# Performance work log

Hardware: AMD Instinct MI355X
Metric: run time of the kernel (lower is better)

## Reference

```python
import jax, jax.numpy as jnp
import numpy as np
import math

EMBED_DIM = 1024
NUM_HEADS = 16
HEAD_DIM = EMBED_DIM // NUM_HEADS


def setup_inputs() -> dict:
    key = jax.random.key(0)
    ks = jax.random.split(key, 5)
    x = jax.random.normal(ks[0], (4, 2048, EMBED_DIM), dtype=jnp.float32)
    # Linear params (torch nn.Linear: y = x @ W.T + b); init scale ~ 1/sqrt(fan_in)
    s = 1.0 / math.sqrt(EMBED_DIM)
    qkv_w = jax.random.uniform(ks[1], (3 * EMBED_DIM, EMBED_DIM), jnp.float32, -s, s)
    qkv_b = jax.random.uniform(ks[2], (3 * EMBED_DIM,), jnp.float32, -s, s)
    proj_w = jax.random.uniform(ks[3], (EMBED_DIM, EMBED_DIM), jnp.float32, -s, s)
    proj_b = jax.random.uniform(ks[4], (EMBED_DIM,), jnp.float32, -s, s)
    return {"x": x, "qkv_w": qkv_w, "qkv_b": qkv_b, "proj_w": proj_w, "proj_b": proj_b}


def reference(x, qkv_w, qkv_b, proj_w, proj_b):
    bsz, num_tokens, dim = x.shape
    qkv = x @ qkv_w.T + qkv_b  # [B, S, 3*D]
    qkv = qkv.reshape(bsz, num_tokens, 3, NUM_HEADS, HEAD_DIM)
    qkv = jnp.transpose(qkv, (2, 0, 3, 1, 4))  # [3, B, H, S, hd]
    q, k, v = qkv[0], qkv[1], qkv[2]
    scale = 1.0 / math.sqrt(HEAD_DIM)
    attn_scores = jnp.einsum('bhqd,bhkd->bhqk', q, k) * scale  # [B, H, S, S]
    attn = jax.nn.softmax(attn_scores, axis=-1)
    out = jnp.einsum('bhqk,bhkd->bhqd', attn, v)  # [B, H, S, hd]
    out = jnp.transpose(out, (0, 2, 1, 3)).reshape(bsz, num_tokens, dim)
    out = out @ proj_w.T + proj_b
    return out
```

## Files before the change

kernel.cpp:

```cpp
#include <hip/hip_runtime.h>
#include <stdint.h>

#define DEVICE static __device__ __forceinline__

typedef __bf16 bf16x8 __attribute__((ext_vector_type(8)));
typedef float f32x4 __attribute__((ext_vector_type(4)));

#define AS1 __attribute__((address_space(1)))
#define AS3 __attribute__((address_space(3)))

DEVICE void g2l16(const void* gptr, void* lptr) {
  __builtin_amdgcn_global_load_lds((AS1 uint32_t*)(uintptr_t)gptr,
                                   (AS3 uint32_t*)(uint32_t)(uintptr_t)lptr,
                                   16, 0, 0);
}

DEVICE float b2f(ushort h) {
  union { uint32_t u; float f; } v;
  v.u = ((uint32_t)h) << 16;
  return v.f;
}
DEVICE ushort f2b(float f) {
  union { float f; uint32_t u; } v;
  v.f = f;
  uint32_t u = v.u;
  return (ushort)((u + 0x7FFFu + ((u >> 16) & 1u)) >> 16);
}

#if defined(__has_builtin) && __has_builtin(__builtin_amdgcn_exp2f)
DEVICE float fast_exp2(float x) { return __builtin_amdgcn_exp2f(x); }
#else
extern "C" __device__ float __ocml_native_exp2_f32(float);
DEVICE float fast_exp2(float x) { return __ocml_native_exp2_f32(x); }
#endif

#define QSCALE 0.1803368801111244f

DEVICE int kperm(int x) {
  return (x & 0x23) | ((x & 0x18) >> 1) | ((x & 0x4) << 2);
}

__global__ void detect_dtype(const ushort* __restrict__ xu, int* __restrict__ flag) {
  __shared__ int bad;
  if (threadIdx.x == 0) bad = 0;
  __syncthreads();
  int mybad = 0;
#pragma unroll
  for (int j = 0; j < 8; ++j) {
    const int i = threadIdx.x * 8 + j;
    const ushort u = xu[2 * i];
    const int e = (u >> 7) & 0xFF;
    if (!(e == 0 || (e >= 96 && e <= 160))) mybad++;
  }
  atomicAdd(&bad, mybad);
  __syncthreads();
  if (threadIdx.x == 0) *flag = (bad > 512) ? 1 : 0;
}

__global__ void convert_bf16(const void* __restrict__ src, ushort* __restrict__ dst,
                             int n, const int* __restrict__ flag) {
  const bool isf32 = (*flag != 0);
  const int n8 = n >> 3;
  for (int i = blockIdx.x * blockDim.x + threadIdx.x; i < n8;
       i += gridDim.x * blockDim.x) {
    ushort pk[8];
    if (isf32) {
      const float4 a = ((const float4*)src)[2 * i];
      const float4 b = ((const float4*)src)[2 * i + 1];
      pk[0] = f2b(a.x); pk[1] = f2b(a.y); pk[2] = f2b(a.z); pk[3] = f2b(a.w);
      pk[4] = f2b(b.x); pk[5] = f2b(b.y); pk[6] = f2b(b.z); pk[7] = f2b(b.w);
      *(uint4*)&dst[8 * i] = *(const uint4*)pk;
    } else {
      *(uint4*)&dst[8 * i] = ((const uint4*)src)[i];
    }
  }
}

template <int MODE, int GN>
__global__ __launch_bounds__(256)
void gemm_bt(const ushort* __restrict__ A, const ushort* __restrict__ W,
             const ushort* __restrict__ bias, ushort* __restrict__ O0,
             ushort* __restrict__ O1, ushort* __restrict__ O2,
             int M, int N, int K, const int* __restrict__ flag)
{
  __shared__ union SM {
    struct { ushort As[128 * 64]; ushort Bs[128 * 64]; } s;
    ushort Ct[128 * 136];
  } sm;

  const int tid = threadIdx.x;
  const int lane = tid & 63;
  const int wave = tid >> 6;
  const int quad = lane >> 4;
  const int lo = lane & 15;

  const int lin = blockIdx.y * gridDim.x + blockIdx.x;
  const int per = GN * gridDim.y;
  const int grp = lin / per;
  const int w   = lin % per;
  const int bxn = grp * GN + (w % GN);
  const int bym = w / GN;
  const int m0 = bym * 128;
  const int n0 = bxn * 128;

  const int wm = (wave >> 1) * 64;
  const int wn = (wave & 1) * 64;

  f32x4 acc[4][4] = {};

  for (int k0 = 0; k0 < K; k0 += 64) {
    __syncthreads();
#pragma unroll
    for (int i = 0; i < 4; ++i) {
      const int c = tid + 256 * i;
      const int row = c >> 3;
      const int kc = (c & 7) << 3;
      g2l16(A + (size_t)(m0 + row) * K + k0 + kc,
            (char*)sm.s.As + ((wave << 6) + (i << 8)) * 16);
      g2l16(W + (size_t)(n0 + row) * K + k0 + kc,
            (char*)sm.s.Bs + ((wave << 6) + (i << 8)) * 16);
    }
    __syncthreads();

#pragma unroll
    for (int ks = 0; ks < 2; ++ks) {
      bf16x8 af[4], bfr[4];
#pragma unroll
      for (int t = 0; t < 4; ++t) {
        af[t]  = *(const bf16x8*)&sm.s.As[(wm + t * 16 + lo) * 64 + ks * 32 + quad * 8];
        bfr[t] = *(const bf16x8*)&sm.s.Bs[(wn + t * 16 + lo) * 64 + ks * 32 + quad * 8];
      }
#pragma unroll
      for (int mt = 0; mt < 4; ++mt)
#pragma unroll
        for (int nt = 0; nt < 4; ++nt)
          acc[mt][nt] = __builtin_amdgcn_mfma_f32_16x16x32_bf16(
              af[mt], bfr[nt], acc[mt][nt], 0, 0, 0);
    }
  }

  if (MODE == 0) {
    const int which = n0 >> 10;
    if (which == 2) {
#pragma unroll
      for (int nt = 0; nt < 4; ++nt) {
        const int n = n0 + wn + nt * 16 + lo;
        const float bv2 = b2f(bias[n]);
        const int h = (n >> 6) & 15;
        const int d = n & 63;
#pragma unroll
        for (int mt = 0; mt < 4; ++mt) {
          const int mb = m0 + wm + mt * 16 + quad * 4;
          const int b = mb >> 11, s0 = mb & 2047;
          ushort pk[4];
#pragma unroll
          for (int r = 0; r < 4; ++r) pk[r] = f2b(acc[mt][nt][r] + bv2);
          *(uint2*)&O2[((size_t)(b * 16 + h) * 64 + d) * 2048 + s0] =
              *(const uint2*)pk;
        }
      }
    } else {
      const float qs = (which == 0) ? QSCALE : 1.0f;
      ushort* __restrict__ dst = (which == 0) ? O0 : O1;
      __syncthreads();
#pragma unroll
      for (int nt = 0; nt < 4; ++nt) {
        const int n = n0 + wn + nt * 16 + lo;
        const float bv2 = b2f(bias[n]);
#pragma unroll
        for (int mt = 0; mt < 4; ++mt)
#pragma unroll
          for (int r = 0; r < 4; ++r)
            sm.Ct[(wm + mt * 16 + quad * 4 + r) * 136 + wn + nt * 16 + lo] =
                f2b((acc[mt][nt][r] + bv2) * qs);
      }
      __syncthreads();
#pragma unroll
      for (int i = 0; i < 8; ++i) {
        const int c = tid + 256 * i;
        const int nch = c & 15;
        const int ml = c >> 4;
        const int n = n0 + nch * 8;
        const int h = (n >> 6) & 15;
        const int d = n & 63;
        const int mg = m0 + ml;
        const int b = mg >> 11;
        int s = mg & 2047;
        if (which == 1) s = (s & ~63) | kperm(s & 63);
        const uint4 val = *(const uint4*)&sm.Ct[ml * 136 + nch * 8];
        *(uint4*)&dst[(((size_t)(b * 16 + h) * 2048 + s) << 6) + d] = val;
      }
    }
  } else {
    const bool f32out = (*flag != 0);
    float* Of = (float*)O0;
#pragma unroll
    for (int nt = 0; nt < 4; ++nt) {
      const int n = n0 + wn + nt * 16 + lo;
      const float bv2 = b2f(bias[n]);
#pragma unroll
      for (int mt = 0; mt < 4; ++mt)
#pragma unroll
        for (int r = 0; r < 4; ++r) {
          const int m = m0 + wm + mt * 16 + quad * 4 + r;
          const float val = acc[mt][nt][r] + bv2;
          if (f32out) Of[(size_t)m * N + n] = val;
          else        O0[(size_t)m * N + n] = f2b(val);
        }
    }
  }
}

__global__ __launch_bounds__(256, 4)
void attn_fwd(const ushort* __restrict__ qp, const ushort* __restrict__ kp,
              const ushort* __restrict__ vp, ushort* __restrict__ o)
{
  __shared__ ushort Qs[128 * 64];
  __shared__ ushort Ks[64 * 64];
  __shared__ ushort Vt[64 * 64];

  const int tid = threadIdx.x;
  const int lane = tid & 63;
  const int wave = tid >> 6;
  const int quad = lane >> 4;
  const int lo = lane & 15;
  const int bh = blockIdx.y;
  const int q0 = blockIdx.x * 128;

  const ushort* Qg = qp + (size_t)bh * 2048 * 64;
  const ushort* Kg = kp + (size_t)bh * 2048 * 64;
  const ushort* Vg = vp + (size_t)bh * 64 * 2048;

#pragma unroll
  for (int i = 0; i < 4; ++i) {
    const int c = tid + 256 * i;
    const int row = c >> 3;
    const int kc = (c & 7) << 3;
    g2l16(Qg + (size_t)(q0 + row) * 64 + kc,
          (char*)Qs + ((wave << 6) + (i << 8)) * 16);
  }
  __syncthreads();

  bf16x8 qf[2][2];
#pragma unroll
  for (int mt = 0; mt < 2; ++mt)
#pragma unroll
    for (int ks = 0; ks < 2; ++ks)
      qf[mt][ks] = *(const bf16x8*)&Qs[(wave * 32 + mt * 16 + lo) * 64 + ks * 32 + quad * 8];

  bf16x8 ones;
#pragma unroll
  for (int j = 0; j < 8; ++j) ones[j] = (__bf16)1.0f;

  f32x4 oacc[2][4] = {};
  f32x4 sumacc[2] = {};

  for (int j0 = 0; j0 < 2048; j0 += 64) {
    __syncthreads();
#pragma unroll
    for (int i = 0; i < 2; ++i) {
      const int c = tid + 256 * i;
      const int row = c >> 3;
      const int kc = (c & 7) << 3;
      g2l16(Kg + (size_t)(j0 + row) * 64 + kc,
            (char*)Ks + ((wave << 6) + (i << 8)) * 16);
      g2l16(Vg + (size_t)row * 2048 + j0 + kc,
            (char*)Vt + ((wave << 6) + (i << 8)) * 16);
    }
    __syncthreads();

    f32x4 sacc[2][4] = {};
#pragma unroll
    for (int ks = 0; ks < 2; ++ks) {
#pragma unroll
      for (int nt = 0; nt < 4; ++nt) {
        const bf16x8 kf = *(const bf16x8*)&Ks[(nt * 16 + lo) * 64 + ks * 32 + quad * 8];
#pragma unroll
        for (int mt = 0; mt < 2; ++mt)
          sacc[mt][nt] = __builtin_amdgcn_mfma_f32_16x16x32_bf16(
              kf, qf[mt][ks], sacc[mt][nt], 0, 0, 0);
      }
    }

    bf16x8 pfr[2][2];
#pragma unroll
    for (int mt = 0; mt < 2; ++mt) {
      float p[4][4];
#pragma unroll
      for (int nt = 0; nt < 4; ++nt)
#pragma unroll
        for (int r = 0; r < 4; ++r)
          p[nt][r] = fast_exp2(sacc[mt][nt][r]);
#pragma unroll
      for (int b = 0; b < 2; ++b)
#pragma unroll
        for (int h = 0; h < 2; ++h)
#pragma unroll
          for (int r = 0; r < 4; ++r)
            pfr[mt][b][4 * h + r] = (__bf16)p[2 * b + h][r];
    }

#pragma unroll
    for (int b = 0; b < 2; ++b) {
#pragma unroll
      for (int mt = 0; mt < 2; ++mt)
        sumacc[mt] = __builtin_amdgcn_mfma_f32_16x16x32_bf16(
            pfr[mt][b], ones, sumacc[mt], 0, 0, 0);
#pragma unroll
      for (int dt = 0; dt < 4; ++dt) {
        const bf16x8 vf = *(const bf16x8*)&Vt[(dt * 16 + lo) * 64 + b * 32 + quad * 8];
#pragma unroll
        for (int mt = 0; mt < 2; ++mt)
          oacc[mt][dt] = __builtin_amdgcn_mfma_f32_16x16x32_bf16(
              pfr[mt][b], vf, oacc[mt][dt], 0, 0, 0);
      }
    }
  }

  const int b_ = bh >> 4;
  const int h = bh & 15;
#pragma unroll
  for (int mt = 0; mt < 2; ++mt) {
#pragma unroll
    for (int r = 0; r < 4; ++r) {
      const float inv = 1.0f / sumacc[mt][r];
      const int srow = q0 + wave * 32 + mt * 16 + quad * 4 + r;
#pragma unroll
      for (int dt = 0; dt < 4; ++dt) {
        o[(((size_t)(b_ * 2048 + srow)) << 10) + h * 64 + dt * 16 + lo] =
            f2b(oacc[mt][dt][r] * inv);
      }
    }
  }
}

extern "C" void kernel_launch(void* const* d_in, const int* in_sizes, int n_in,
                              void* d_out, int out_size, void* d_ws, size_t ws_size,
                              hipStream_t stream) {
  const size_t N_X  = (size_t)4 * 2048 * 1024;
  const size_t N_WQ = (size_t)3072 * 1024;
  const size_t N_BQ = 3072;
  const size_t N_WP = (size_t)1024 * 1024;
  const size_t N_BP = 1024;
  const size_t HSD  = (size_t)64 * 2048 * 64;

  ushort* xb = (ushort*)d_ws;
  ushort* wq = xb + N_X;
  ushort* bq = wq + N_WQ;
  ushort* wp = bq + N_BQ;
  ushort* bp = wp + N_WP;
  ushort* qb = bp + N_BP;
  ushort* kb = qb + HSD;
  ushort* vb = kb + HSD;
  ushort* ab = vb + HSD;
  int* flag  = (int*)(ab + HSD);

  detect_dtype<<<1, 256, 0, stream>>>((const ushort*)d_in[0], flag);
  convert_bf16<<<1024, 256, 0, stream>>>(d_in[0], xb, (int)N_X, flag);
  convert_bf16<<<512, 256, 0, stream>>>(d_in[1], wq, (int)N_WQ, flag);
  convert_bf16<<<2, 256, 0, stream>>>(d_in[2], bq, (int)N_BQ, flag);
  convert_bf16<<<256, 256, 0, stream>>>(d_in[3], wp, (int)N_WP, flag);
  convert_bf16<<<1, 256, 0, stream>>>(d_in[4], bp, (int)N_BP, flag);

  gemm_bt<0, 6><<<dim3(24, 64), dim3(256), 0, stream>>>(
      xb, wq, bq, qb, kb, vb, 8192, 3072, 1024, flag);
  attn_fwd<<<dim3(16, 64), dim3(256), 0, stream>>>(qb, kb, vb, ab);
  gemm_bt<1, 4><<<dim3(8, 64), dim3(256), 0, stream>>>(
      ab, wp, bp, (ushort*)d_out, nullptr, nullptr, 8192, 1024, 1024, flag);
}
```

Measured before the change: 299.3 us.

## Map GEMM tiles to XCD-local rectangles and double attention KV tile

```diff
diff --git a/kernel.cpp b/kernel.cpp
--- a/kernel.cpp
+++ b/kernel.cpp
@@ -76,7 +76,7 @@
   }
 }
 
-template <int MODE, int GN>
+template <int MODE, int RM, int RN>
 __global__ __launch_bounds__(256)
 void gemm_bt(const ushort* __restrict__ A, const ushort* __restrict__ W,
              const ushort* __restrict__ bias, ushort* __restrict__ O0,
@@ -95,13 +95,15 @@
   const int lo = lane & 15;
 
   const int lin = blockIdx.y * gridDim.x + blockIdx.x;
-  const int per = GN * gridDim.y;
-  const int grp = lin / per;
-  const int w   = lin % per;
-  const int bxn = grp * GN + (w % GN);
-  const int bym = w / GN;
-  const int m0 = bym * 128;
-  const int n0 = bxn * 128;
+  const int xcd = lin & 7;
+  const int slot = lin >> 3;
+  const int rects_n = gridDim.x / RN;
+  const int rn = xcd % rects_n;
+  const int rm = xcd / rects_n;
+  const int ml = slot / RN;
+  const int nl = slot % RN;
+  const int m0 = (rm * RM + ml) * 128;
+  const int n0 = (rn * RN + nl) * 128;
 
   const int wm = (wave >> 1) * 64;
   const int wn = (wave & 1) * 64;
@@ -179,15 +181,15 @@
       for (int i = 0; i < 8; ++i) {
         const int c = tid + 256 * i;
         const int nch = c & 15;
-        const int ml = c >> 4;
+        const int ml2 = c >> 4;
         const int n = n0 + nch * 8;
         const int h = (n >> 6) & 15;
         const int d = n & 63;
-        const int mg = m0 + ml;
+        const int mg = m0 + ml2;
         const int b = mg >> 11;
         int s = mg & 2047;
         if (which == 1) s = (s & ~63) | kperm(s & 63);
-        const uint4 val = *(const uint4*)&sm.Ct[ml * 136 + nch * 8];
+        const uint4 val = *(const uint4*)&sm.Ct[ml2 * 136 + nch * 8];
         *(uint4*)&dst[(((size_t)(b * 16 + h) * 2048 + s) << 6) + d] = val;
       }
     }
@@ -216,8 +218,8 @@
               const ushort* __restrict__ vp, ushort* __restrict__ o)
 {
   __shared__ ushort Qs[128 * 64];
-  __shared__ ushort Ks[64 * 64];
-  __shared__ ushort Vt[64 * 64];
+  __shared__ ushort Ks[128 * 64];
+  __shared__ ushort Vt[64 * 128];
 
   const int tid = threadIdx.x;
   const int lane = tid & 63;
@@ -255,64 +257,69 @@
   f32x4 oacc[2][4] = {};
   f32x4 sumacc[2] = {};
 
-  for (int j0 = 0; j0 < 2048; j0 += 64) {
+  for (int j0 = 0; j0 < 2048; j0 += 128) {
     __syncthreads();
 #pragma unroll
-    for (int i = 0; i < 2; ++i) {
+    for (int i = 0; i < 4; ++i) {
       const int c = tid + 256 * i;
-      const int row = c >> 3;
-      const int kc = (c & 7) << 3;
-      g2l16(Kg + (size_t)(j0 + row) * 64 + kc,
+      const int krow = c >> 3, kcol = (c & 7) << 3;
+      g2l16(Kg + (size_t)(j0 + krow) * 64 + kcol,
             (char*)Ks + ((wave << 6) + (i << 8)) * 16);
-      g2l16(Vg + (size_t)row * 2048 + j0 + kc,
+      const int vrow = c >> 4, vcol = (c & 15) << 3;
+      g2l16(Vg + (size_t)vrow * 2048 + j0 + vcol,
             (char*)Vt + ((wave << 6) + (i << 8)) * 16);
     }
     __syncthreads();
 
-    f32x4 sacc[2][4] = {};
-#pragma unroll
-    for (int ks = 0; ks < 2; ++ks) {
-#pragma unroll
-      for (int nt = 0; nt < 4; ++nt) {
-        const bf16x8 kf = *(const bf16x8*)&Ks[(nt * 16 + lo) * 64 + ks * 32 + quad * 8];
+#pragma unroll
+    for (int half = 0; half < 2; ++half) {
+      f32x4 sacc[2][4] = {};
+#pragma unroll
+      for (int ks = 0; ks < 2; ++ks) {
+#pragma unroll
+        for (int nt = 0; nt < 4; ++nt) {
+          const bf16x8 kf =
+              *(const bf16x8*)&Ks[(half * 64 + nt * 16 + lo) * 64 + ks * 32 + quad * 8];
+#pragma unroll
+          for (int mt = 0; mt < 2; ++mt)
+            sacc[mt][nt] = __builtin_amdgcn_mfma_f32_16x16x32_bf16(
+                kf, qf[mt][ks], sacc[mt][nt], 0, 0, 0);
+        }
+      }
+
+      bf16x8 pfr[2][2];
+#pragma unroll
+      for (int mt = 0; mt < 2; ++mt) {
+        float p[4][4];
+#pragma unroll
+        for (int nt = 0; nt < 4; ++nt)
+#pragma unroll
+          for (int r = 0; r < 4; ++r)
+            p[nt][r] = fast_exp2(sacc[mt][nt][r]);
+#pragma unroll
+        for (int b = 0; b < 2; ++b)
+#pragma unroll
+          for (int h = 0; h < 2; ++h)
+#pragma unroll
+            for (int r = 0; r < 4; ++r)
+              pfr[mt][b][4 * h + r] = (__bf16)p[2 * b + h][r];
+      }
+
+#pragma unroll
+      for (int b = 0; b < 2; ++b) {
 #pragma unroll
         for (int mt = 0; mt < 2; ++mt)
-          sacc[mt][nt] = __builtin_amdgcn_mfma_f32_16x16x32_bf16(
-              kf, qf[mt][ks], sacc[mt][nt], 0, 0, 0);
-      }
-    }
-
-    bf16x8 pfr[2][2];
-#pragma unroll
-    for (int mt = 0; mt < 2; ++mt) {
-      float p[4][4];
-#pragma unroll
-      for (int nt = 0; nt < 4; ++nt)
-#pragma unroll
-        for (int r = 0; r < 4; ++r)
-          p[nt][r] = fast_exp2(sacc[mt][nt][r]);
-#pragma unroll
-      for (int b = 0; b < 2; ++b)
-#pragma unroll
-        for (int h = 0; h < 2; ++h)
-#pragma unroll
-          for (int r = 0; r < 4; ++r)
-            pfr[mt][b][4 * h + r] = (__bf16)p[2 * b + h][r];
-    }
-
-#pragma unroll
-    for (int b = 0; b < 2; ++b) {
-#pragma unroll
-      for (int mt = 0; mt < 2; ++mt)
-        sumacc[mt] = __builtin_amdgcn_mfma_f32_16x16x32_bf16(
-            pfr[mt][b], ones, sumacc[mt], 0, 0, 0);
-#pragma unroll
-      for (int dt = 0; dt < 4; ++dt) {
-        const bf16x8 vf = *(const bf16x8*)&Vt[(dt * 16 + lo) * 64 + b * 32 + quad * 8];
-#pragma unroll
-        for (int mt = 0; mt < 2; ++mt)
-          oacc[mt][dt] = __builtin_amdgcn_mfma_f32_16x16x32_bf16(
-              pfr[mt][b], vf, oacc[mt][dt], 0, 0, 0);
+          sumacc[mt] = __builtin_amdgcn_mfma_f32_16x16x32_bf16(
+              pfr[mt][b], ones, sumacc[mt], 0, 0, 0);
+#pragma unroll
+        for (int dt = 0; dt < 4; ++dt) {
+          const bf16x8 vf =
+              *(const bf16x8*)&Vt[(dt * 16 + lo) * 128 + half * 64 + b * 32 + quad * 8];
+#pragma unroll
+          for (int mt = 0; mt < 2; ++mt)
+            oacc[mt][dt] = __builtin_amdgcn_mfma_f32_16x16x32_bf16(
+                pfr[mt][b], vf, oacc[mt][dt], 0, 0, 0);
+        }
       }
     }
   }
@@ -362,9 +369,9 @@
   convert_bf16<<<256, 256, 0, stream>>>(d_in[3], wp, (int)N_WP, flag);
   convert_bf16<<<1, 256, 0, stream>>>(d_in[4], bp, (int)N_BP, flag);
 
-  gemm_bt<0, 6><<<dim3(24, 64), dim3(256), 0, stream>>>(
+  gemm_bt<0, 16, 12><<<dim3(24, 64), dim3(256), 0, stream>>>(
       xb, wq, bq, qb, kb, vb, 8192, 3072, 1024, flag);
   attn_fwd<<<dim3(16, 64), dim3(256), 0, stream>>>(qb, kb, vb, ab);
-  gemm_bt<1, 4><<<dim3(8, 64), dim3(256), 0, stream>>>(
+  gemm_bt<1, 8, 8><<<dim3(8, 64), dim3(256), 0, stream>>>(
       ab, wp, bp, (ushort*)d_out, nullptr, nullptr, 8192, 1024, 1024, flag);
 }
```

After: 335.6 us. 12.2% more time.
